# Optimization experiments

Measured on AMD Instinct MI355X. Metric: run time of the kernel, lower is better.

The kernel has to match this reference:

```python
import jax, jax.numpy as jnp
import numpy as np

E = 7          # ensemble_size
STATE = 32
ACTION = 8
HID = [256, 256, 256, 128]
B = 32768


def _init_linear(key, e, fan_in, fan_out):
    kw, kb = jax.random.split(key)
    bound = 1.0 / np.sqrt(fan_in)
    W = jax.random.uniform(kw, (e, fan_in, fan_out), jnp.float32, -bound, bound)
    b = jax.random.uniform(kb, (e, fan_out), jnp.float32, -bound, bound)
    return W, b


def setup_inputs() -> dict:
    key = jax.random.key(0)
    ks = jax.random.split(key, 9)
    state = jax.random.normal(ks[0], (B, STATE), jnp.float32)
    action = jax.random.normal(ks[1], (B, ACTION), jnp.float32)
    dims = [STATE + ACTION] + HID
    W0, b0 = _init_linear(ks[2], E, dims[0], dims[1])
    W1, b1 = _init_linear(ks[3], E, dims[1], dims[2])
    W2, b2 = _init_linear(ks[4], E, dims[2], dims[3])
    W3, b3 = _init_linear(ks[5], E, dims[3], dims[4])
    Wmu, bmu = _init_linear(ks[6], E, dims[4], STATE)
    Wsig, bsig = _init_linear(ks[7], E, dims[4], STATE)
    max_logstd = jnp.ones((STATE,), jnp.float32)
    min_logstd = jnp.full((STATE,), -5.0, jnp.float32)
    return {
        'state': state, 'action': action,
        'W0': W0, 'b0': b0, 'W1': W1, 'b1': b1,
        'W2': W2, 'b2': b2, 'W3': W3, 'b3': b3,
        'Wmu': Wmu, 'bmu': bmu, 'Wsig': Wsig, 'bsig': bsig,
        'max_logstd': max_logstd, 'min_logstd': min_logstd,
    }


def _swish(x):
    return x * jax.nn.sigmoid(x)


def _soft_clamp(x, _min, _max):
    x = _max - jax.nn.softplus(_max - x)
    x = _min + jax.nn.softplus(x - _min)
    return x


def reference(state, action, W0, b0, W1, b1, W2, b2, W3, b3,
              Wmu, bmu, Wsig, bsig, max_logstd, min_logstd):
    # Broadcast inputs to the ensemble axis: [E, B, D]
    x = jnp.concatenate([state, action], axis=-1)            # [B, S+A]
    h = jnp.broadcast_to(x, (E,) + x.shape)                   # [E, B, S+A]
    # Batched per-ensemble GEMM chain (grouped GEMM)
    h = _swish(jnp.einsum('ebi,eio->ebo', h, W0) + b0[:, None, :])
    h = _swish(jnp.einsum('ebi,eio->ebo', h, W1) + b1[:, None, :])
    h = _swish(jnp.einsum('ebi,eio->ebo', h, W2) + b2[:, None, :])
    h = _swish(jnp.einsum('ebi,eio->ebo', h, W3) + b3[:, None, :])
    mu = jnp.einsum('ebi,eio->ebo', h, Wmu) + bmu[:, None, :]         # [E, B, S]
    log_sigma = jnp.einsum('ebi,eio->ebo', h, Wsig) + bsig[:, None, :]
    log_sigma = _soft_clamp(log_sigma, min_logstd, max_logstd)
    sigma = jnp.exp(log_sigma)
    mu = mu + state[None, :, :]                                        # residual
    return mu, sigma
```

## Files before the change

kernel.cpp:

```cpp
#include <hip/hip_runtime.h>
#include <math.h>
#include <stdint.h>

#define E_N     7
#define BATCH   32768
#define STATE_D 32
#define ACT_D   8
#define DOUT    32

typedef _Float16 f16;
typedef __attribute__((ext_vector_type(4)))  _Float16 f16x4;
typedef __attribute__((ext_vector_type(8)))  _Float16 f16x8;
typedef __attribute__((ext_vector_type(16))) float    f32x16;

#define OFF_L0  0
#define OFF_L1  114688
#define OFF_L2  573440
#define OFF_L3  1032192
#define OFF_H   1261568
#define WS_ELEMS 1318912
#define WS_NEED  ((size_t)WS_ELEMS*2)

__device__ __forceinline__ float swish_f(float x) {
    float t = __expf(-x);
    return x * __builtin_amdgcn_rcpf(1.0f + t);
}
__device__ __forceinline__ float softplus_fast(float z) {
    float sp = __logf(1.0f + __expf(z));
    return (z > 20.0f) ? z : sp;
}
__device__ __forceinline__ float soft_clamp_f(float x, float mn, float mx) {
    x = mx - softplus_fast(mx - x);
    x = mn + softplus_fast(x - mn);
    return x;
}

#define PREP_THREADS 164864
__global__ __launch_bounds__(256) void prep_f16(
    const float* __restrict__ W0, const float* __restrict__ W1,
    const float* __restrict__ W2, const float* __restrict__ W3,
    const float* __restrict__ Wmu, const float* __restrict__ Wsg,
    unsigned short* __restrict__ ws)
{
    int t = blockIdx.x * 256 + threadIdx.x;
    if (t >= PREP_THREADS) return;
    int slice = t >> 6, l = t & 63;
    int l31 = l & 31, lg = l >> 5;
    const float* src; int e, nt, kt, Ksrc, N; bool head = false;
    if (slice < 224)       { int r = slice;      e=r>>5; r&=31;  nt=r>>2; kt=r&3;  src=W0; Ksrc=40;  N=256; }
    else if (slice < 1120) { int r = slice-224;  e=r>>7; r&=127; nt=r>>4; kt=r&15; src=W1; Ksrc=256; N=256; }
    else if (slice < 2016) { int r = slice-1120; e=r>>7; r&=127; nt=r>>4; kt=r&15; src=W2; Ksrc=256; N=256; }
    else if (slice < 2464) { int r = slice-2016; e=r>>6; r&=63;  nt=r>>4; kt=r&15; src=W3; Ksrc=256; N=128; }
    else                   { int r = slice-2464; e=r>>4; r&=15;  nt=r>>3; kt=r&7;
                             src = (nt==0) ? Wmu : Wsg; Ksrc=128; N=32; head=true; }
    int n  = head ? l31 : nt*32 + l31;
    int k0 = kt*16 + lg*8;
    f16x8 v;
    #pragma unroll
    for (int j = 0; j < 8; ++j) {
        int k = k0 + j;
        float x = (k < Ksrc) ? src[(e*Ksrc + k)*N + n] : 0.0f;
        v[j] = (f16)x;
    }
    *reinterpret_cast<f16x8*>(ws + (size_t)slice*512 + l*8) = v;
}

template<int KT, int NTW, int ASTR, int SWZM>
__device__ __forceinline__ void layer_sw(
    const unsigned short* __restrict__ Wf, const float* __restrict__ bias,
    const unsigned short* __restrict__ aBuf, unsigned short* __restrict__ dBuf,
    int nt0, int lane)
{
    const int l31 = lane & 31, lg = lane >> 5;
    f32x16 acc[2][NTW];
    #pragma unroll
    for (int mt = 0; mt < 2; ++mt)
        #pragma unroll
        for (int jj = 0; jj < NTW; ++jj)
            #pragma unroll
            for (int r = 0; r < 16; ++r) acc[mt][jj][r] = 0.0f;

    const int ab0 = l31*ASTR, ab1 = (32 + l31)*ASTR;
    const int sw0 = l31 & SWZM, sw1 = (32 + l31) & SWZM;

    #pragma unroll
    for (int kt = 0; kt < KT; ++kt) {
        const int kg = kt*2 + lg;
        f16x8 w[NTW];
        #pragma unroll
        for (int jj = 0; jj < NTW; ++jj)
            w[jj] = *reinterpret_cast<const f16x8*>(Wf + (nt0+jj)*KT*512 + kt*512 + lane*8);
        f16x8 a0 = *reinterpret_cast<const f16x8*>(aBuf + ab0 + ((kg ^ sw0) << 3));
        f16x8 a1 = *reinterpret_cast<const f16x8*>(aBuf + ab1 + ((kg ^ sw1) << 3));
        #pragma unroll
        for (int jj = 0; jj < NTW; ++jj) {
            acc[0][jj] = __builtin_amdgcn_mfma_f32_32x32x16_f16(w[jj], a0, acc[0][jj], 0, 0, 0);
            acc[1][jj] = __builtin_amdgcn_mfma_f32_32x32x16_f16(w[jj], a1, acc[1][jj], 0, 0, 0);
        }
    }
    __syncthreads();
    #pragma unroll
    for (int mt = 0; mt < 2; ++mt) {
        const int m  = mt*32 + l31;
        const int rb = m*256, swd = m & 15;
        #pragma unroll
        for (int jj = 0; jj < NTW; ++jj) {
            const int nb = (nt0+jj)*32 + 4*lg;
            #pragma unroll
            for (int g = 0; g < 4; ++g) {
                float4 bv = *reinterpret_cast<const float4*>(&bias[nb + 8*g]);
                f16x4 pk;
                pk[0] = (f16)swish_f(acc[mt][jj][4*g+0] + bv.x);
                pk[1] = (f16)swish_f(acc[mt][jj][4*g+1] + bv.y);
                pk[2] = (f16)swish_f(acc[mt][jj][4*g+2] + bv.z);
                pk[3] = (f16)swish_f(acc[mt][jj][4*g+3] + bv.w);
                const int cg = (nt0+jj)*4 + g;
                *reinterpret_cast<f16x4*>(dBuf + rb + ((cg ^ swd) << 3) + 4*lg) = pk;
            }
        }
    }
    __syncthreads();
}

template<int NTW>
__device__ __forceinline__ void layer0_direct(
    const unsigned short* __restrict__ Wf, const float* __restrict__ bias,
    const float* __restrict__ gs, const float* __restrict__ ga,
    unsigned short* __restrict__ dBuf, int brow0, int nt0, int lane)
{
    const int l31 = lane & 31, lg = lane >> 5;
    #pragma unroll
    for (int mt = 0; mt < 2; ++mt) {
        const int row = brow0 + mt*32 + l31;
        f16x8 xf[3];
        #pragma unroll
        for (int kt = 0; kt < 2; ++kt) {
            const float* p = &gs[(size_t)row*STATE_D + kt*16 + lg*8];
            float4 q0 = *reinterpret_cast<const float4*>(p);
            float4 q1 = *reinterpret_cast<const float4*>(p + 4);
            f16x8 v;
            v[0]=(f16)q0.x; v[1]=(f16)q0.y; v[2]=(f16)q0.z; v[3]=(f16)q0.w;
            v[4]=(f16)q1.x; v[5]=(f16)q1.y; v[6]=(f16)q1.z; v[7]=(f16)q1.w;
            xf[kt] = v;
        }
        {
            f16x8 v;
            if (lg == 0) {
                const float* p = &ga[(size_t)row*ACT_D];
                float4 q0 = *reinterpret_cast<const float4*>(p);
                float4 q1 = *reinterpret_cast<const float4*>(p + 4);
                v[0]=(f16)q0.x; v[1]=(f16)q0.y; v[2]=(f16)q0.z; v[3]=(f16)q0.w;
                v[4]=(f16)q1.x; v[5]=(f16)q1.y; v[6]=(f16)q1.z; v[7]=(f16)q1.w;
            } else {
                #pragma unroll
                for (int i = 0; i < 8; ++i) v[i] = (f16)0.0f;
            }
            xf[2] = v;
        }
        f32x16 acc[NTW];
        #pragma unroll
        for (int jj = 0; jj < NTW; ++jj)
            #pragma unroll
            for (int r = 0; r < 16; ++r) acc[jj][r] = 0.0f;
        #pragma unroll
        for (int kt = 0; kt < 3; ++kt) {
            #pragma unroll
            for (int jj = 0; jj < NTW; ++jj) {
                f16x8 w = *reinterpret_cast<const f16x8*>(Wf + (nt0+jj)*4*512 + kt*512 + lane*8);
                acc[jj] = __builtin_amdgcn_mfma_f32_32x32x16_f16(w, xf[kt], acc[jj], 0, 0, 0);
            }
        }
        const int m  = mt*32 + l31;
        const int rb = m*256, swd = m & 15;
        #pragma unroll
        for (int jj = 0; jj < NTW; ++jj) {
            const int nb = (nt0+jj)*32 + 4*lg;
            #pragma unroll
            for (int g = 0; g < 4; ++g) {
                float4 bv = *reinterpret_cast<const float4*>(&bias[nb + 8*g]);
                f16x4 pk;
                pk[0] = (f16)swish_f(acc[jj][4*g+0] + bv.x);
                pk[1] = (f16)swish_f(acc[jj][4*g+1] + bv.y);
                pk[2] = (f16)swish_f(acc[jj][4*g+2] + bv.z);
                pk[3] = (f16)swish_f(acc[jj][4*g+3] + bv.w);
                const int cg = (nt0+jj)*4 + g;
                *reinterpret_cast<f16x4*>(dBuf + rb + ((cg ^ swd) << 3) + 4*lg) = pk;
            }
        }
    }
    __syncthreads();
}

__global__ __launch_bounds__(256, 3) void ens16(
    const float* __restrict__ gs, const float* __restrict__ ga,
    const unsigned short* __restrict__ ws,
    const float* __restrict__ b0, const float* __restrict__ b1,
    const float* __restrict__ b2, const float* __restrict__ b3,
    const float* __restrict__ bmu, const float* __restrict__ bsg,
    const float* __restrict__ mxl, const float* __restrict__ mnl,
    float* __restrict__ out)
{
    __shared__ unsigned short hbuf[64*256];

    const int tid = threadIdx.x, lane = tid & 63, wv = tid >> 6;
    const int e = blockIdx.x >> 9;
    const int brow0 = (blockIdx.x & 511) << 6;

    layer0_direct<2>(ws + OFF_L0 + e*16384, b0 + e*256, gs, ga, hbuf, brow0, wv*2, lane);
    layer_sw<16,2, 256,15>(ws + OFF_L1 + e*65536, b1 + e*256, hbuf, hbuf, wv*2, lane);
    layer_sw<16,2, 256,15>(ws + OFF_L2 + e*65536, b2 + e*256, hbuf, hbuf, wv*2, lane);
    layer_sw<16,1, 256,15>(ws + OFF_L3 + e*32768, b3 + e*128, hbuf, hbuf, wv,   lane);

    {
        const unsigned short* WH = ws + OFF_H + e*8192;
        const int mt = wv >> 1, ntH = wv & 1;
        const int l31 = lane & 31, lg = lane >> 5;
        float bvH = (ntH == 0) ? bmu[e*32 + l31] : bsg[e*32 + l31];
        f32x16 acc;
        #pragma unroll
        for (int r = 0; r < 16; ++r) acc[r] = bvH;
        const unsigned short* wpH = WH + ntH*8*512 + lane*8;
        const int row0 = mt*32 + l31, ab = row0*256, sw = row0 & 15;
        #pragma unroll
        for (int kt = 0; kt < 8; ++kt) {
            int kg = kt*2 + lg;
            f16x8 ac = *reinterpret_cast<const f16x8*>(hbuf + ab + ((kg ^ sw) << 3));
            f16x8 bc = *reinterpret_cast<const f16x8*>(wpH + kt*512);
            acc = __builtin_amdgcn_mfma_f32_32x32x16_f16(ac, bc, acc, 0, 0, 0);
        }
        if (ntH == 0) {
            #pragma unroll
            for (int r = 0; r < 16; ++r) {
                int grow = brow0 + mt*32 + (r & 3) + 8*(r >> 2) + 4*lg;
                float v = acc[r] + gs[(size_t)grow*32 + l31];
                __builtin_nontemporal_store(v, &out[((size_t)e*BATCH + grow)*32 + l31]);
            }
        } else {
            float mx = mxl[l31], mn = mnl[l31];
            #pragma unroll
            for (int r = 0; r < 16; ++r) {
                int grow = brow0 + mt*32 + (r & 3) + 8*(r >> 2) + 4*lg;
                float v = __expf(soft_clamp_f(acc[r], mn, mx));
                __builtin_nontemporal_store(v,
                    &out[(size_t)E_N*BATCH*32 + ((size_t)e*BATCH + grow)*32 + l31]);
            }
        }
    }
}

#define TILE_B  64
#define THREADS 256
#define LDH     260
#define LDX     44
__device__ __forceinline__ float f4c(const float4& v, int i) {
    return reinterpret_cast<const float*>(&v)[i];
}
__device__ __forceinline__ float softplus_ref(float z) {
    return (z > 20.0f) ? z : log1pf(expf(z));
}
__device__ __forceinline__ float soft_clamp_ref(float x, float mn, float mx) {
    x = mx - softplus_ref(mx - x);
    x = mn + softplus_ref(x - mn);
    return x;
}
template<int K, int N, int LDIN, bool SW>
__device__ __forceinline__ void layer_fn(const float* __restrict__ lin,
                                         float* __restrict__ lout,
                                         const float* __restrict__ W,
                                         const float* __restrict__ bias,
                                         int tx, int ty)
{
    constexpr int CH = N / 64;
    float4 acc[4][CH];
    #pragma unroll
    for (int jj = 0; jj < CH; ++jj) {
        float4 bv = *reinterpret_cast<const float4*>(&bias[jj*64 + tx*4]);
        #pragma unroll
        for (int r = 0; r < 4; ++r) acc[r][jj] = bv;
    }
    for (int k0 = 0; k0 < K; k0 += 4) {
        float4 a[4];
        #pragma unroll
        for (int r = 0; r < 4; ++r)
            a[r] = *reinterpret_cast<const float4*>(&lin[(ty*4 + r)*LDIN + k0]);
        #pragma unroll
        for (int kk = 0; kk < 4; ++kk) {
            float4 w[CH];
            #pragma unroll
            for (int jj = 0; jj < CH; ++jj)
                w[jj] = *reinterpret_cast<const float4*>(&W[(k0+kk)*N + jj*64 + tx*4]);
            #pragma unroll
            for (int r = 0; r < 4; ++r) {
                float av = f4c(a[r], kk);
                #pragma unroll
                for (int jj = 0; jj < CH; ++jj) {
                    acc[r][jj].x = fmaf(av, w[jj].x, acc[r][jj].x);
                    acc[r][jj].y = fmaf(av, w[jj].y, acc[r][jj].y);
                    acc[r][jj].z = fmaf(av, w[jj].z, acc[r][jj].z);
                    acc[r][jj].w = fmaf(av, w[jj].w, acc[r][jj].w);
                }
            }
        }
    }
    __syncthreads();
    #pragma unroll
    for (int r = 0; r < 4; ++r) {
        #pragma unroll
        for (int jj = 0; jj < CH; ++jj) {
            float4 v = acc[r][jj];
            if (SW) { v.x = swish_f(v.x); v.y = swish_f(v.y); v.z = swish_f(v.z); v.w = swish_f(v.w); }
            *reinterpret_cast<float4*>(&lout[(ty*4 + r)*LDH + jj*64 + tx*4]) = v;
        }
    }
    __syncthreads();
}
__global__ __launch_bounds__(THREADS, 2)
void ens_fwd(const float* __restrict__ g_state, const float* __restrict__ g_action,
             const float* __restrict__ W0, const float* __restrict__ b0,
             const float* __restrict__ W1, const float* __restrict__ b1,
             const float* __restrict__ W2, const float* __restrict__ b2,
             const float* __restrict__ W3, const float* __restrict__ b3,
             const float* __restrict__ Wmu, const float* __restrict__ bmu,
             const float* __restrict__ Wsg, const float* __restrict__ bsg,
             const float* __restrict__ mxl, const float* __restrict__ mnl,
             float* __restrict__ out)
{
    __shared__ float h[TILE_B * LDH];
    __shared__ float xb[TILE_B * LDX];
    const int tid  = threadIdx.x;
    const int tx   = tid & 15;
    const int ty   = tid >> 4;
    const int e    = blockIdx.x / (BATCH / TILE_B);
    const int brow0 = (blockIdx.x % (BATCH / TILE_B)) * TILE_B;
    for (int i = tid; i < TILE_B * 8; i += THREADS) {
        int r = i >> 3, c = (i & 7) << 2;
        *reinterpret_cast<float4*>(&xb[r*LDX + c]) =
            *reinterpret_cast<const float4*>(&g_state[(size_t)(brow0 + r)*STATE_D + c]);
    }
    if (tid < TILE_B * 2) {
        int r = tid >> 1, c = (tid & 1) << 2;
        *reinterpret_cast<float4*>(&xb[r*LDX + STATE_D + c]) =
            *reinterpret_cast<const float4*>(&g_action[(size_t)(brow0 + r)*ACT_D + c]);
    }
    __syncthreads();
    layer_fn<40,  256, LDX, true>(xb, h, W0 + e*40*256,  b0 + e*256, tx, ty);
    layer_fn<256, 256, LDH, true>(h,  h, W1 + e*256*256, b1 + e*256, tx, ty);
    layer_fn<256, 256, LDH, true>(h,  h, W2 + e*256*256, b2 + e*256, tx, ty);
    layer_fn<256, 128, LDH, true>(h,  h, W3 + e*256*128, b3 + e*128, tx, ty);
    const float* Wm = Wmu + e*128*32;
    const float* Ws = Wsg + e*128*32;
    float2 am[4], as[4];
    {
        float2 bm = *reinterpret_cast<const float2*>(&bmu[e*32 + tx*2]);
        float2 bs = *reinterpret_cast<const float2*>(&bsg[e*32 + tx*2]);
        #pragma unroll
        for (int r = 0; r < 4; ++r) { am[r] = bm; as[r] = bs; }
    }
    for (int k0 = 0; k0 < 128; k0 += 4) {
        float4 a[4];
        #pragma unroll
        for (int r = 0; r < 4; ++r)
            a[r] = *reinterpret_cast<const float4*>(&h[(ty*4 + r)*LDH + k0]);
        #pragma unroll
        for (int kk = 0; kk < 4; ++kk) {
            float2 wm = *reinterpret_cast<const float2*>(&Wm[(k0+kk)*32 + tx*2]);
            float2 ws2 = *reinterpret_cast<const float2*>(&Ws[(k0+kk)*32 + tx*2]);
            #pragma unroll
            for (int r = 0; r < 4; ++r) {
                float av = f4c(a[r], kk);
                am[r].x = fmaf(av, wm.x, am[r].x);
                am[r].y = fmaf(av, wm.y, am[r].y);
                as[r].x = fmaf(av, ws2.x, as[r].x);
                as[r].y = fmaf(av, ws2.y, as[r].y);
            }
        }
    }
    const float2 mx = *reinterpret_cast<const float2*>(&mxl[tx*2]);
    const float2 mn = *reinterpret_cast<const float2*>(&mnl[tx*2]);
    #pragma unroll
    for (int r = 0; r < 4; ++r) {
        const int row = brow0 + ty*4 + r;
        float2 st = *reinterpret_cast<const float2*>(&g_state[(size_t)row*STATE_D + tx*2]);
        float2 mu; mu.x = am[r].x + st.x; mu.y = am[r].y + st.y;
        float2 sg;
        sg.x = expf(soft_clamp_ref(as[r].x, mn.x, mx.x));
        sg.y = expf(soft_clamp_ref(as[r].y, mn.y, mx.y));
        size_t idx = ((size_t)e*BATCH + row)*DOUT + tx*2;
        *reinterpret_cast<float2*>(&out[idx]) = mu;
        *reinterpret_cast<float2*>(&out[(size_t)E_N*BATCH*DOUT + idx]) = sg;
    }
}

extern "C" void kernel_launch(void* const* d_in, const int* in_sizes, int n_in,
                              void* d_out, int out_size, void* d_ws, size_t ws_size,
                              hipStream_t stream) {
    (void)in_sizes; (void)n_in; (void)out_size;
    const float* state  = (const float*)d_in[0];
    const float* action = (const float*)d_in[1];
    const float* W0  = (const float*)d_in[2];
    const float* b0  = (const float*)d_in[3];
    const float* W1  = (const float*)d_in[4];
    const float* b1  = (const float*)d_in[5];
    const float* W2  = (const float*)d_in[6];
    const float* b2  = (const float*)d_in[7];
    const float* W3  = (const float*)d_in[8];
    const float* b3  = (const float*)d_in[9];
    const float* Wmu = (const float*)d_in[10];
    const float* bmu = (const float*)d_in[11];
    const float* Wsg = (const float*)d_in[12];
    const float* bsg = (const float*)d_in[13];
    const float* mxl = (const float*)d_in[14];
    const float* mnl = (const float*)d_in[15];
    float* out = (float*)d_out;

    if (ws_size >= WS_NEED) {
        unsigned short* ws = (unsigned short*)d_ws;
        prep_f16<<<dim3((PREP_THREADS + 255)/256), dim3(256), 0, stream>>>(
            W0, W1, W2, W3, Wmu, Wsg, ws);
        ens16<<<dim3(E_N * 512), dim3(256), 0, stream>>>(
            state, action, ws, b0, b1, b2, b3, bmu, bsg, mxl, mnl, out);
    } else {
        ens_fwd<<<dim3(E_N * (BATCH/TILE_B)), dim3(THREADS), 0, stream>>>(
            state, action, W0, b0, W1, b1, W2, b2, W3, b3,
            Wmu, bmu, Wsg, bsg, mxl, mnl, out);
    }
}
```

Before: 225.1 us.

## Split each 64-row tile across 8 waves with one M-tile per wave

The block grows from 4 to 8 waves (512 threads). Each wave now handles one 32-row M-tile and a pair of N-tiles, instead of both M-tiles, which halves the accumulator registers per wave. The aim is more waves per CU and better latency hiding. In exchange, each weight fragment is loaded from global memory twice per block, once per M-tile wave, and half the waves sit idle during the output head.

```diff
diff --git a/kernel.cpp b/kernel.cpp
--- a/kernel.cpp
+++ b/kernel.cpp
@@ -66,110 +66,34 @@
 }
 
 template<int KT, int NTW, int ASTR, int SWZM>
-__device__ __forceinline__ void layer_sw(
+__device__ __forceinline__ void layer_sw8(
     const unsigned short* __restrict__ Wf, const float* __restrict__ bias,
     const unsigned short* __restrict__ aBuf, unsigned short* __restrict__ dBuf,
-    int nt0, int lane)
+    int nt0, int mt, int lane)
 {
     const int l31 = lane & 31, lg = lane >> 5;
-    f32x16 acc[2][NTW];
-    #pragma unroll
-    for (int mt = 0; mt < 2; ++mt)
-        #pragma unroll
-        for (int jj = 0; jj < NTW; ++jj)
-            #pragma unroll
-            for (int r = 0; r < 16; ++r) acc[mt][jj][r] = 0.0f;
-
-    const int ab0 = l31*ASTR, ab1 = (32 + l31)*ASTR;
-    const int sw0 = l31 & SWZM, sw1 = (32 + l31) & SWZM;
+    f32x16 acc[NTW];
+    #pragma unroll
+    for (int jj = 0; jj < NTW; ++jj)
+        #pragma unroll
+        for (int r = 0; r < 16; ++r) acc[jj][r] = 0.0f;
+
+    const int arow = mt*32 + l31;
+    const int ab = arow * ASTR;
+    const int sw = arow & SWZM;
 
     #pragma unroll
     for (int kt = 0; kt < KT; ++kt) {
         const int kg = kt*2 + lg;
-        f16x8 w[NTW];
-        #pragma unroll
-        for (int jj = 0; jj < NTW; ++jj)
-            w[jj] = *reinterpret_cast<const f16x8*>(Wf + (nt0+jj)*KT*512 + kt*512 + lane*8);
-        f16x8 a0 = *reinterpret_cast<const f16x8*>(aBuf + ab0 + ((kg ^ sw0) << 3));
-        f16x8 a1 = *reinterpret_cast<const f16x8*>(aBuf + ab1 + ((kg ^ sw1) << 3));
+        f16x8 a = *reinterpret_cast<const f16x8*>(aBuf + ab + ((kg ^ sw) << 3));
         #pragma unroll
         for (int jj = 0; jj < NTW; ++jj) {
-            acc[0][jj] = __builtin_amdgcn_mfma_f32_32x32x16_f16(w[jj], a0, acc[0][jj], 0, 0, 0);
-            acc[1][jj] = __builtin_amdgcn_mfma_f32_32x32x16_f16(w[jj], a1, acc[1][jj], 0, 0, 0);
-        }
-    }
-    __syncthreads();
-    #pragma unroll
-    for (int mt = 0; mt < 2; ++mt) {
-        const int m  = mt*32 + l31;
-        const int rb = m*256, swd = m & 15;
-        #pragma unroll
-        for (int jj = 0; jj < NTW; ++jj) {
-            const int nb = (nt0+jj)*32 + 4*lg;
-            #pragma unroll
-            for (int g = 0; g < 4; ++g) {
-                float4 bv = *reinterpret_cast<const float4*>(&bias[nb + 8*g]);
-                f16x4 pk;
-                pk[0] = (f16)swish_f(acc[mt][jj][4*g+0] + bv.x);
-                pk[1] = (f16)swish_f(acc[mt][jj][4*g+1] + bv.y);
-                pk[2] = (f16)swish_f(acc[mt][jj][4*g+2] + bv.z);
-                pk[3] = (f16)swish_f(acc[mt][jj][4*g+3] + bv.w);
-                const int cg = (nt0+jj)*4 + g;
-                *reinterpret_cast<f16x4*>(dBuf + rb + ((cg ^ swd) << 3) + 4*lg) = pk;
-            }
-        }
-    }
-    __syncthreads();
-}
-
-template<int NTW>
-__device__ __forceinline__ void layer0_direct(
-    const unsigned short* __restrict__ Wf, const float* __restrict__ bias,
-    const float* __restrict__ gs, const float* __restrict__ ga,
-    unsigned short* __restrict__ dBuf, int brow0, int nt0, int lane)
-{
-    const int l31 = lane & 31, lg = lane >> 5;
-    #pragma unroll
-    for (int mt = 0; mt < 2; ++mt) {
-        const int row = brow0 + mt*32 + l31;
-        f16x8 xf[3];
-        #pragma unroll
-        for (int kt = 0; kt < 2; ++kt) {
-            const float* p = &gs[(size_t)row*STATE_D + kt*16 + lg*8];
-            float4 q0 = *reinterpret_cast<const float4*>(p);
-            float4 q1 = *reinterpret_cast<const float4*>(p + 4);
-            f16x8 v;
-            v[0]=(f16)q0.x; v[1]=(f16)q0.y; v[2]=(f16)q0.z; v[3]=(f16)q0.w;
-            v[4]=(f16)q1.x; v[5]=(f16)q1.y; v[6]=(f16)q1.z; v[7]=(f16)q1.w;
-            xf[kt] = v;
-        }
-        {
-            f16x8 v;
-            if (lg == 0) {
-                const float* p = &ga[(size_t)row*ACT_D];
-                float4 q0 = *reinterpret_cast<const float4*>(p);
-                float4 q1 = *reinterpret_cast<const float4*>(p + 4);
-                v[0]=(f16)q0.x; v[1]=(f16)q0.y; v[2]=(f16)q0.z; v[3]=(f16)q0.w;
-                v[4]=(f16)q1.x; v[5]=(f16)q1.y; v[6]=(f16)q1.z; v[7]=(f16)q1.w;
-            } else {
-                #pragma unroll
-                for (int i = 0; i < 8; ++i) v[i] = (f16)0.0f;
-            }
-            xf[2] = v;
-        }
-        f32x16 acc[NTW];
-        #pragma unroll
-        for (int jj = 0; jj < NTW; ++jj)
-            #pragma unroll
-            for (int r = 0; r < 16; ++r) acc[jj][r] = 0.0f;
-        #pragma unroll
-        for (int kt = 0; kt < 3; ++kt) {
-            #pragma unroll
-            for (int jj = 0; jj < NTW; ++jj) {
-                f16x8 w = *reinterpret_cast<const f16x8*>(Wf + (nt0+jj)*4*512 + kt*512 + lane*8);
-                acc[jj] = __builtin_amdgcn_mfma_f32_32x32x16_f16(w, xf[kt], acc[jj], 0, 0, 0);
-            }
-        }
+            f16x8 w = *reinterpret_cast<const f16x8*>(Wf + (nt0+jj)*KT*512 + kt*512 + lane*8);
+            acc[jj] = __builtin_amdgcn_mfma_f32_32x32x16_f16(w, a, acc[jj], 0, 0, 0);
+        }
+    }
+    __syncthreads();
+    {
         const int m  = mt*32 + l31;
         const int rb = m*256, swd = m & 15;
         #pragma unroll
@@ -191,7 +115,75 @@
     __syncthreads();
 }
 
-__global__ __launch_bounds__(256, 3) void ens16(
+template<int NTW>
+__device__ __forceinline__ void layer0_direct8(
+    const unsigned short* __restrict__ Wf, const float* __restrict__ bias,
+    const float* __restrict__ gs, const float* __restrict__ ga,
+    unsigned short* __restrict__ dBuf, int brow0, int nt0, int mt, int lane)
+{
+    const int l31 = lane & 31, lg = lane >> 5;
+    const int row = brow0 + mt*32 + l31;
+    f16x8 xf[3];
+    #pragma unroll
+    for (int kt = 0; kt < 2; ++kt) {
+        const float* p = &gs[(size_t)row*STATE_D + kt*16 + lg*8];
+        float4 q0 = *reinterpret_cast<const float4*>(p);
+        float4 q1 = *reinterpret_cast<const float4*>(p + 4);
+        f16x8 v;
+        v[0]=(f16)q0.x; v[1]=(f16)q0.y; v[2]=(f16)q0.z; v[3]=(f16)q0.w;
+        v[4]=(f16)q1.x; v[5]=(f16)q1.y; v[6]=(f16)q1.z; v[7]=(f16)q1.w;
+        xf[kt] = v;
+    }
+    {
+        f16x8 v;
+        if (lg == 0) {
+            const float* p = &ga[(size_t)row*ACT_D];
+            float4 q0 = *reinterpret_cast<const float4*>(p);
+            float4 q1 = *reinterpret_cast<const float4*>(p + 4);
+            v[0]=(f16)q0.x; v[1]=(f16)q0.y; v[2]=(f16)q0.z; v[3]=(f16)q0.w;
+            v[4]=(f16)q1.x; v[5]=(f16)q1.y; v[6]=(f16)q1.z; v[7]=(f16)q1.w;
+        } else {
+            #pragma unroll
+            for (int i = 0; i < 8; ++i) v[i] = (f16)0.0f;
+        }
+        xf[2] = v;
+    }
+    f32x16 acc[NTW];
+    #pragma unroll
+    for (int jj = 0; jj < NTW; ++jj)
+        #pragma unroll
+        for (int r = 0; r < 16; ++r) acc[jj][r] = 0.0f;
+    #pragma unroll
+    for (int kt = 0; kt < 3; ++kt) {
+        #pragma unroll
+        for (int jj = 0; jj < NTW; ++jj) {
+            f16x8 w = *reinterpret_cast<const f16x8*>(Wf + (nt0+jj)*4*512 + kt*512 + lane*8);
+            acc[jj] = __builtin_amdgcn_mfma_f32_32x32x16_f16(w, xf[kt], acc[jj], 0, 0, 0);
+        }
+    }
+    {
+        const int m  = mt*32 + l31;
+        const int rb = m*256, swd = m & 15;
+        #pragma unroll
+        for (int jj = 0; jj < NTW; ++jj) {
+            const int nb = (nt0+jj)*32 + 4*lg;
+            #pragma unroll
+            for (int g = 0; g < 4; ++g) {
+                float4 bv = *reinterpret_cast<const float4*>(&bias[nb + 8*g]);
+                f16x4 pk;
+                pk[0] = (f16)swish_f(acc[jj][4*g+0] + bv.x);
+                pk[1] = (f16)swish_f(acc[jj][4*g+1] + bv.y);
+                pk[2] = (f16)swish_f(acc[jj][4*g+2] + bv.z);
+                pk[3] = (f16)swish_f(acc[jj][4*g+3] + bv.w);
+                const int cg = (nt0+jj)*4 + g;
+                *reinterpret_cast<f16x4*>(dBuf + rb + ((cg ^ swd) << 3) + 4*lg) = pk;
+            }
+        }
+    }
+    __syncthreads();
+}
+
+__global__ __launch_bounds__(512, 4) void ens16(
     const float* __restrict__ gs, const float* __restrict__ ga,
     const unsigned short* __restrict__ ws,
     const float* __restrict__ b0, const float* __restrict__ b1,
@@ -205,22 +197,25 @@
     const int tid = threadIdx.x, lane = tid & 63, wv = tid >> 6;
     const int e = blockIdx.x >> 9;
     const int brow0 = (blockIdx.x & 511) << 6;
-
-    layer0_direct<2>(ws + OFF_L0 + e*16384, b0 + e*256, gs, ga, hbuf, brow0, wv*2, lane);
-    layer_sw<16,2, 256,15>(ws + OFF_L1 + e*65536, b1 + e*256, hbuf, hbuf, wv*2, lane);
-    layer_sw<16,2, 256,15>(ws + OFF_L2 + e*65536, b2 + e*256, hbuf, hbuf, wv*2, lane);
-    layer_sw<16,1, 256,15>(ws + OFF_L3 + e*32768, b3 + e*128, hbuf, hbuf, wv,   lane);
-
+    const int mt  = wv & 1;
+    const int ntp = wv >> 1;
+
+    layer0_direct8<2>(ws + OFF_L0 + e*16384, b0 + e*256, gs, ga, hbuf, brow0, ntp*2, mt, lane);
+    layer_sw8<16,2, 256,15>(ws + OFF_L1 + e*65536, b1 + e*256, hbuf, hbuf, ntp*2, mt, lane);
+    layer_sw8<16,2, 256,15>(ws + OFF_L2 + e*65536, b2 + e*256, hbuf, hbuf, ntp*2, mt, lane);
+    layer_sw8<16,1, 256,15>(ws + OFF_L3 + e*32768, b3 + e*128, hbuf, hbuf, ntp,  mt, lane);
+
+    if (wv >= 4) return;
     {
         const unsigned short* WH = ws + OFF_H + e*8192;
-        const int mt = wv >> 1, ntH = wv & 1;
+        const int mtH = wv >> 1, ntH = wv & 1;
         const int l31 = lane & 31, lg = lane >> 5;
         float bvH = (ntH == 0) ? bmu[e*32 + l31] : bsg[e*32 + l31];
         f32x16 acc;
         #pragma unroll
         for (int r = 0; r < 16; ++r) acc[r] = bvH;
         const unsigned short* wpH = WH + ntH*8*512 + lane*8;
-        const int row0 = mt*32 + l31, ab = row0*256, sw = row0 & 15;
+        const int row0 = mtH*32 + l31, ab = row0*256, sw = row0 & 15;
         #pragma unroll
         for (int kt = 0; kt < 8; ++kt) {
             int kg = kt*2 + lg;
@@ -231,7 +226,7 @@
         if (ntH == 0) {
             #pragma unroll
             for (int r = 0; r < 16; ++r) {
-                int grow = brow0 + mt*32 + (r & 3) + 8*(r >> 2) + 4*lg;
+                int grow = brow0 + mtH*32 + (r & 3) + 8*(r >> 2) + 4*lg;
                 float v = acc[r] + gs[(size_t)grow*32 + l31];
                 __builtin_nontemporal_store(v, &out[((size_t)e*BATCH + grow)*32 + l31]);
             }
@@ -239,7 +234,7 @@
             float mx = mxl[l31], mn = mnl[l31];
             #pragma unroll
             for (int r = 0; r < 16; ++r) {
-                int grow = brow0 + mt*32 + (r & 3) + 8*(r >> 2) + 4*lg;
+                int grow = brow0 + mtH*32 + (r & 3) + 8*(r >> 2) + 4*lg;
                 float v = __expf(soft_clamp_f(acc[r], mn, mx));
                 __builtin_nontemporal_store(v,
                     &out[(size_t)E_N*BATCH*32 + ((size_t)e*BATCH + grow)*32 + l31]);
@@ -417,7 +412,7 @@
         unsigned short* ws = (unsigned short*)d_ws;
         prep_f16<<<dim3((PREP_THREADS + 255)/256), dim3(256), 0, stream>>>(
             W0, W1, W2, W3, Wmu, Wsg, ws);
-        ens16<<<dim3(E_N * 512), dim3(256), 0, stream>>>(
+        ens16<<<dim3(E_N * 512), dim3(512), 0, stream>>>(
             state, action, ws, b0, b1, b2, b3, bmu, bsg, mxl, mnl, out);
     } else {
         ens_fwd<<<dim3(E_N * (BATCH/TILE_B)), dim3(THREADS), 0, stream>>>(
```

Result: slower. 247.3 us (+9.8%).
